# Optimization experiments

Measured on AMD Instinct MI355X. Metric: run time of the kernel, lower is better.

## Reference

```python
import jax, jax.numpy as jnp
import numpy as np

B, T, F = 16384, 48, 4
UNITS = 256
OUT_STEPS = 24


def setup_inputs() -> dict:
    key = jax.random.key(0)
    ks = jax.random.split(key, 6)
    s_x = 1.0 / np.sqrt(F)
    s_h = 1.0 / np.sqrt(UNITS)
    return {
        "x": jax.random.normal(ks[0], (B, T, F), jnp.float32),
        "Wx": jax.random.normal(ks[1], (F, 4 * UNITS), jnp.float32) * s_x,
        "Wh": jax.random.normal(ks[2], (UNITS, 4 * UNITS), jnp.float32) * s_h,
        "b": jnp.zeros((4 * UNITS,), jnp.float32),
        "Wd": jax.random.normal(ks[3], (UNITS, F), jnp.float32) * s_h,
        "bd": jnp.zeros((F,), jnp.float32),
    }


def _lstm_cell(xt, h, c, Wx, Wh, b):
    # Keras LSTMCell gate order: i, f, g(cell candidate), o
    z = xt @ Wx + h @ Wh + b  # [B, 4*units]
    i, f, g, o = jnp.split(z, 4, axis=-1)
    i = jax.nn.sigmoid(i)
    f = jax.nn.sigmoid(f)
    g = jnp.tanh(g)
    o = jax.nn.sigmoid(o)
    c_new = f * c + i * g
    h_new = o * jnp.tanh(c_new)
    return h_new, c_new


def reference(x, Wx, Wh, b, Wd, bd):
    bsz = x.shape[0]
    h0 = jnp.zeros((bsz, UNITS), x.dtype)
    c0 = jnp.zeros((bsz, UNITS), x.dtype)

    # --- warmup: run LSTM over the input window, keep final state ---
    def warm_step(carry, xt):
        h, c = carry
        h, c = _lstm_cell(xt, h, c, Wx, Wh, b)
        return (h, c), None

    (h, c), _ = jax.lax.scan(warm_step, (h0, c0), jnp.swapaxes(x, 0, 1))
    pred0 = h @ Wd + bd  # first prediction [B, F]

    def ar_step(carry, _):
        h, c, pred = carry
        h, c = _lstm_cell(pred, h, c, Wx, Wh, b)
        pred = h @ Wd + bd
        return (h, c, pred), pred

    _, preds = jax.lax.scan(ar_step, (h, c, pred0), None, length=OUT_STEPS - 1)
    preds = jnp.concatenate([pred0[None], preds], axis=0)  # [out_steps, B, F]
    return jnp.swapaxes(preds, 0, 1)  # [B, out_steps, F]
```

## Files before the change

kernel.cpp:

```cpp
#include <hip/hip_runtime.h>


typedef unsigned short u16;
typedef __attribute__((ext_vector_type(8))) short bf16x8;
typedef __attribute__((ext_vector_type(16))) float f32x16;

#define PITCH 296
#define HB 18944
#define WARM 48
#define STEPS 71
#define LOG2E  1.442695041f
#define LOG2E2 2.885390082f

__device__ __forceinline__ u16 f2bf(float f) {
    unsigned u = __float_as_uint(f);
    u += 0x7FFFu + ((u >> 16) & 1u);
    return (u16)(u >> 16);
}

__device__ __forceinline__ unsigned pk_bf16(float a, float b) {
    unsigned d;
    asm("v_cvt_pk_bf16_f32 %0, %1, %2" : "=v"(d) : "v"(a), "v"(b));
    return d;
}

__device__ __forceinline__ void sync_lds() {
    asm volatile("s_waitcnt lgkmcnt(0)\n\ts_barrier" ::: "memory");
}

__global__ void prep_weights(const float* __restrict__ Wx,
                             const float* __restrict__ Wh,
                             const float* __restrict__ b,
                             const float* __restrict__ Wd,
                             const float* __restrict__ bd,
                             u16* __restrict__ whext,
                             u16* __restrict__ wdp) {
    int idx = blockIdx.x * 256 + threadIdx.x;
    if (idx < 36864) {
        int lane = idx & 63;
        int frag = idx >> 6;
        int wv = frag & 7;
        int g = (frag >> 3) & 3;
        int kt = frag >> 5;
        int k0 = kt * 16 + (lane >> 5) * 8;
        int n = 256 * g + 32 * wv + (lane & 31);
        float sc = (g == 2) ? LOG2E2 : LOG2E;
        u16 v[8];
#pragma unroll
        for (int j = 0; j < 8; ++j) {
            int k = k0 + j;
            float f = 0.0f;
            if (k < 256) f = Wh[k * 1024 + n];
            else if (k < 260) f = Wx[(k - 256) * 1024 + n];
            else if (k == 260) f = b[n];
            v[j] = f2bf(f * sc);
        }
        ushort4* dst = (ushort4*)(whext + (size_t)idx * 8);
        dst[0] = make_ushort4(v[0], v[1], v[2], v[3]);
        dst[1] = make_ushort4(v[4], v[5], v[6], v[7]);
    } else if (idx < 36864 + 1152) {
        int id2 = idx - 36864;
        int lane = id2 & 63;
        int kt = id2 >> 6;
        int k0 = kt * 16 + (lane >> 5) * 8;
        int f_ = lane & 31;
        u16 v[8];
#pragma unroll
        for (int j = 0; j < 8; ++j) {
            int k = k0 + j;
            float f = 0.0f;
            if (f_ < 4) {
                if (k < 256) f = Wd[k * 4 + f_];
                else if (k == 260) f = bd[f_];
            }
            v[j] = f2bf(f);
        }
        ushort4* dst = (ushort4*)(wdp + (size_t)id2 * 8);
        dst[0] = make_ushort4(v[0], v[1], v[2], v[3]);
        dst[1] = make_ushort4(v[4], v[5], v[6], v[7]);
    }
}

#define WLOADT(DST, T) do {                                                   \
    const char* _wk = wp + ((size_t)(T) << 15);                               \
    _Pragma("unroll") for (int g = 0; g < 4; ++g)                             \
        DST[g] = *(const bf16x8*)(_wk + voff[g]);                             \
} while (0)

#define HLOADT(DST, T) do {                                                   \
    DST[0] = *(const bf16x8*)&hr[hrow0 + (T) * 16];                           \
    DST[1] = *(const bf16x8*)&hr[hrow1 + (T) * 16];                           \
} while (0)

#define MT(WA, HBX)                                                           \
    _Pragma("unroll") for (int m = 0; m < 2; ++m)                             \
    _Pragma("unroll") for (int g = 0; g < 4; ++g)                             \
        acc[m][g] = __builtin_amdgcn_mfma_f32_32x32x16_bf16(                  \
            WA[g], HBX[m], acc[m][g], 0, 0, 0);

__global__ __launch_bounds__(512, 2) void lstm_main(
    const float* __restrict__ x, const u16* __restrict__ whext,
    const u16* __restrict__ wdp, float* __restrict__ out) {
    __shared__ __align__(16) u16 hbuf[2 * HB];

    const int tid = threadIdx.x;
    const int w = tid >> 6;
    const int l = tid & 63;
    const int l31 = l & 31;
    const int lh = l >> 5;
    const long long rowBase = (long long)blockIdx.x * 64;

    {
        int4 z = make_int4(0, 0, 0, 0);
        for (int i = tid; i < 4736; i += 512) ((int4*)hbuf)[i] = z;
    }
    sync_lds();
    if (tid < 64) {
        hbuf[tid * PITCH + 260] = (u16)0x3F80;
        hbuf[HB + tid * PITCH + 260] = (u16)0x3F80;
        const float4 xv = *(const float4*)(x + (rowBase + tid) * 192);
        uint2* p = (uint2*)&hbuf[tid * PITCH + 256];
        *p = make_uint2(pk_bf16(xv.x, xv.y), pk_bf16(xv.z, xv.w));
    }

    const char* __restrict__ wp = (const char*)whext;
    const char* __restrict__ dp = (const char*)wdp;
    int voff[4];
#pragma unroll
    for (int g = 0; g < 4; ++g) voff[g] = ((g * 8 + w) * 64 + l) * 16;
    const int hrow0 = l31 * PITCH + lh * 8;
    const int hrow1 = (32 + l31) * PITCH + lh * 8;

    f32x16 c[2] = {};
    bf16x8 awA[4], awB[4];
    WLOADT(awA, 0);
    WLOADT(awB, 1);

    for (int step = 0; step < STEPS; ++step) {
        const u16* hr = hbuf + (step & 1) * HB;
        u16* hw = hbuf + ((step & 1) ^ 1) * HB;

        float4 xv = make_float4(0.f, 0.f, 0.f, 0.f);
        if (w == 0 && step < WARM - 1)
            xv = *(const float4*)(x + (rowBase + l) * 192 + (step + 1) * 4);

        sync_lds();

        f32x16 acc[2][4] = {};
        bf16x8 hbA[2], hbB[2];
        HLOADT(hbA, 0);
        HLOADT(hbB, 1);

#pragma unroll 1
        for (int t = 0; t < 13; t += 2) {
            MT(awA, hbA);
            WLOADT(awA, t + 2); HLOADT(hbA, t + 2);
            MT(awB, hbB);
            WLOADT(awB, t + 3); HLOADT(hbB, t + 3);
        }
        MT(awA, hbA);
        WLOADT(awA, 16); HLOADT(hbA, 16);
        MT(awB, hbB);
        WLOADT(awB, 1);
        MT(awA, hbA);
        WLOADT(awA, 0);

#pragma unroll
        for (int m = 0; m < 2; ++m) {
            const int hwrow = (32 * m + l31) * PITCH + 32 * w + 4 * lh;
#pragma unroll
            for (int q = 0; q < 4; ++q) {
                unsigned pk[2];
#pragma unroll
                for (int hp = 0; hp < 2; ++hp) {
                    float h2[2];
#pragma unroll
                    for (int rr = 0; rr < 2; ++rr) {
                        const int r = q * 4 + hp * 2 + rr;
                        float ei = __builtin_amdgcn_exp2f(-acc[m][0][r]);
                        float ef = __builtin_amdgcn_exp2f(-acc[m][1][r]);
                        float eg = __builtin_amdgcn_exp2f(-acc[m][2][r]);
                        float eo = __builtin_amdgcn_exp2f(-acc[m][3][r]);
                        float ai = 1.0f + ei, af = 1.0f + ef;
                        float ag = 1.0f + eg, ao = 1.0f + eo;
                        float P  = ai * ag;
                        float rD = __builtin_amdgcn_rcpf(P * af);
                        float cn = fmaf(c[m][r] * P, rD, (1.0f - eg) * af * rD);
                        c[m][r] = cn;
                        float ec = __builtin_amdgcn_exp2f(-LOG2E2 * cn);
                        float rE = __builtin_amdgcn_rcpf(ao * (1.0f + ec));
                        h2[rr] = (1.0f - ec) * rE;
                    }
                    pk[hp] = pk_bf16(h2[0], h2[1]);
                }
                *(uint2*)&hw[hwrow + 8 * q] = make_uint2(pk[0], pk[1]);
            }
        }

        if (step < WARM - 1) {
            if (w == 0) {
                uint2* p = (uint2*)&hw[l * PITCH + 256];
                *p = make_uint2(pk_bf16(xv.x, xv.y), pk_bf16(xv.z, xv.w));
            }
        } else {
            sync_lds();
            if (w < 2) {
                f32x16 pacc = {};
                const int prow = (32 * w + l31) * PITCH + lh * 8;
#pragma unroll
                for (int kt = 0; kt < 17; ++kt) {
                    bf16x8 hbp = *(const bf16x8*)&hw[prow + kt * 16];
                    bf16x8 wap = *(const bf16x8*)(dp + ((size_t)kt * 64 + l) * 16);
                    pacc = __builtin_amdgcn_mfma_f32_32x32x16_bf16(wap, hbp, pacc, 0, 0, 0);
                }
                if (lh == 0) {
                    int s = step - (WARM - 1);
                    int batch = 32 * w + l31;
                    *(float4*)&out[((rowBase + batch) * 24 + s) * 4] =
                        make_float4(pacc[0], pacc[1], pacc[2], pacc[3]);
                    *(uint2*)&hw[batch * PITCH + 256] =
                        make_uint2(pk_bf16(pacc[0], pacc[1]), pk_bf16(pacc[2], pacc[3]));
                }
            }
        }
    }
}

extern "C" void kernel_launch(void* const* d_in, const int* in_sizes, int n_in,
                              void* d_out, int out_size, void* d_ws, size_t ws_size,
                              hipStream_t stream) {
    const float* x  = (const float*)d_in[0];
    const float* Wx = (const float*)d_in[1];
    const float* Wh = (const float*)d_in[2];
    const float* b  = (const float*)d_in[3];
    const float* Wd = (const float*)d_in[4];
    const float* bd = (const float*)d_in[5];
    float* out = (float*)d_out;

    u16* whext = (u16*)d_ws;
    u16* wdp = (u16*)((char*)d_ws + 589824);

    prep_weights<<<(36864 + 1152 + 255) / 256, 256, 0, stream>>>(Wx, Wh, b, Wd, bd, whext, wdp);
    lstm_main<<<256, 512, 0, stream>>>(x, whext, wdp, out);
}
```

Baseline: 751.1 us.

## Triple-buffer weight fragments, make per-wave weight layout contiguous, use 16x16 MFMA for dense head

The prepared weight layout is reordered so each wave's four gate fragments for a k-tile sit contiguously, and the padded k-tiles drop from 18 to 17. The main k-loop goes from double to triple buffering of weight registers, issuing loads two stages ahead to hide global/L2 latency behind MFMAs. The output projection now uses 16x16x32 MFMAs across four waves instead of 32x32x16 across two, which cuts the wasted padded columns and the serial chain length. The third buffer adds register pressure under the 2-blocks-per-CU launch bound.

```diff
diff --git a/kernel.cpp b/kernel.cpp
--- a/kernel.cpp
+++ b/kernel.cpp
@@ -3,6 +3,7 @@
 
 typedef unsigned short u16;
 typedef __attribute__((ext_vector_type(8))) short bf16x8;
+typedef __attribute__((ext_vector_type(4))) float f32x4;
 typedef __attribute__((ext_vector_type(16))) float f32x16;
 
 #define PITCH 296
@@ -36,12 +37,12 @@
                              u16* __restrict__ whext,
                              u16* __restrict__ wdp) {
     int idx = blockIdx.x * 256 + threadIdx.x;
-    if (idx < 36864) {
+    if (idx < 34816) {
         int lane = idx & 63;
-        int frag = idx >> 6;
-        int wv = frag & 7;
-        int g = (frag >> 3) & 3;
-        int kt = frag >> 5;
+        int fr = idx >> 6;
+        int g = fr & 3;
+        int wv = (fr >> 2) & 7;
+        int kt = fr >> 5;
         int k0 = kt * 16 + (lane >> 5) * 8;
         int n = 256 * g + 32 * wv + (lane & 31);
         float sc = (g == 2) ? LOG2E2 : LOG2E;
@@ -58,20 +59,20 @@
         ushort4* dst = (ushort4*)(whext + (size_t)idx * 8);
         dst[0] = make_ushort4(v[0], v[1], v[2], v[3]);
         dst[1] = make_ushort4(v[4], v[5], v[6], v[7]);
-    } else if (idx < 36864 + 1152) {
-        int id2 = idx - 36864;
+    } else if (idx < 34816 + 576) {
+        int id2 = idx - 34816;
         int lane = id2 & 63;
-        int kt = id2 >> 6;
-        int k0 = kt * 16 + (lane >> 5) * 8;
-        int f_ = lane & 31;
+        int kc = id2 >> 6;
+        int m = lane & 15;
+        int k0 = kc * 32 + (lane >> 4) * 8;
         u16 v[8];
 #pragma unroll
         for (int j = 0; j < 8; ++j) {
             int k = k0 + j;
             float f = 0.0f;
-            if (f_ < 4) {
-                if (k < 256) f = Wd[k * 4 + f_];
-                else if (k == 260) f = bd[f_];
+            if (m < 4) {
+                if (k < 256) f = Wd[k * 4 + m];
+                else if (k == 260) f = bd[m];
             }
             v[j] = f2bf(f);
         }
@@ -81,13 +82,15 @@
     }
 }
 
-#define WLOADT(DST, T) do {                                                   \
-    const char* _wk = wp + ((size_t)(T) << 15);                               \
-    _Pragma("unroll") for (int g = 0; g < 4; ++g)                             \
-        DST[g] = *(const bf16x8*)(_wk + voff[g]);                             \
+#define WL(DST, T) do {                                                       \
+    const char* _p = wpw + ((size_t)(T) << 15);                               \
+    DST[0] = *(const bf16x8*)(_p + voffl);                                    \
+    DST[1] = *(const bf16x8*)(_p + voffl + 1024);                             \
+    DST[2] = *(const bf16x8*)(_p + voffl + 2048);                             \
+    DST[3] = *(const bf16x8*)(_p + voffl + 3072);                             \
 } while (0)
 
-#define HLOADT(DST, T) do {                                                   \
+#define HL(DST, T) do {                                                       \
     DST[0] = *(const bf16x8*)&hr[hrow0 + (T) * 16];                           \
     DST[1] = *(const bf16x8*)&hr[hrow1 + (T) * 16];                           \
 } while (0)
@@ -97,6 +100,8 @@
     _Pragma("unroll") for (int g = 0; g < 4; ++g)                             \
         acc[m][g] = __builtin_amdgcn_mfma_f32_32x32x16_bf16(                  \
             WA[g], HBX[m], acc[m][g], 0, 0, 0);
+
+#define STG(K, AW, HBX) do { MT(AW, HBX); WL(AW, (K) + 3); HL(HBX, (K) + 2); } while (0)
 
 __global__ __launch_bounds__(512, 2) void lstm_main(
     const float* __restrict__ x, const u16* __restrict__ whext,
@@ -123,18 +128,17 @@
         *p = make_uint2(pk_bf16(xv.x, xv.y), pk_bf16(xv.z, xv.w));
     }
 
-    const char* __restrict__ wp = (const char*)whext;
+    const char* __restrict__ wpw = (const char*)whext + (size_t)w * 4096;
     const char* __restrict__ dp = (const char*)wdp;
-    int voff[4];
-#pragma unroll
-    for (int g = 0; g < 4; ++g) voff[g] = ((g * 8 + w) * 64 + l) * 16;
+    const int voffl = l * 16;
     const int hrow0 = l31 * PITCH + lh * 8;
     const int hrow1 = (32 + l31) * PITCH + lh * 8;
 
     f32x16 c[2] = {};
-    bf16x8 awA[4], awB[4];
-    WLOADT(awA, 0);
-    WLOADT(awB, 1);
+    bf16x8 aw0[4], aw1[4], aw2[4];
+    WL(aw0, 0);
+    WL(aw1, 1);
+    WL(aw2, 2);
 
     for (int step = 0; step < STEPS; ++step) {
         const u16* hr = hbuf + (step & 1) * HB;
@@ -147,23 +151,24 @@
         sync_lds();
 
         f32x16 acc[2][4] = {};
-        bf16x8 hbA[2], hbB[2];
-        HLOADT(hbA, 0);
-        HLOADT(hbB, 1);
-
+        bf16x8 hb0[2], hb1[2];
+        HL(hb0, 0);
+        HL(hb1, 1);
+
+        STG(0, aw0, hb0);
+        STG(1, aw1, hb1);
 #pragma unroll 1
-        for (int t = 0; t < 13; t += 2) {
-            MT(awA, hbA);
-            WLOADT(awA, t + 2); HLOADT(hbA, t + 2);
-            MT(awB, hbB);
-            WLOADT(awB, t + 3); HLOADT(hbB, t + 3);
-        }
-        MT(awA, hbA);
-        WLOADT(awA, 16); HLOADT(hbA, 16);
-        MT(awB, hbB);
-        WLOADT(awB, 1);
-        MT(awA, hbA);
-        WLOADT(awA, 0);
+        for (int k = 2; k < 14; k += 6) {
+            STG(k + 0, aw2, hb0);
+            STG(k + 1, aw0, hb1);
+            STG(k + 2, aw1, hb0);
+            STG(k + 3, aw2, hb1);
+            STG(k + 4, aw0, hb0);
+            STG(k + 5, aw1, hb1);
+        }
+        MT(aw2, hb0); WL(aw2, 2); HL(hb0, 16);
+        MT(aw0, hb1); WL(aw0, 0);
+        MT(aw1, hb0); WL(aw1, 1);
 
 #pragma unroll
         for (int m = 0; m < 2; ++m) {
@@ -204,18 +209,19 @@
             }
         } else {
             sync_lds();
-            if (w < 2) {
-                f32x16 pacc = {};
-                const int prow = (32 * w + l31) * PITCH + lh * 8;
-#pragma unroll
-                for (int kt = 0; kt < 17; ++kt) {
-                    bf16x8 hbp = *(const bf16x8*)&hw[prow + kt * 16];
-                    bf16x8 wap = *(const bf16x8*)(dp + ((size_t)kt * 64 + l) * 16);
-                    pacc = __builtin_amdgcn_mfma_f32_32x32x16_bf16(wap, hbp, pacc, 0, 0, 0);
+            if (w < 4) {
+                f32x4 pacc = {};
+                const int col = l & 15;
+                const int prow = (16 * w + col) * PITCH + (l >> 4) * 8;
+#pragma unroll
+                for (int kc = 0; kc < 9; ++kc) {
+                    bf16x8 hbp = *(const bf16x8*)&hw[prow + kc * 32];
+                    bf16x8 wap = *(const bf16x8*)(dp + ((size_t)kc * 64 + l) * 16);
+                    pacc = __builtin_amdgcn_mfma_f32_16x16x32_bf16(wap, hbp, pacc, 0, 0, 0);
                 }
-                if (lh == 0) {
+                if ((l >> 4) == 0) {
                     int s = step - (WARM - 1);
-                    int batch = 32 * w + l31;
+                    int batch = 16 * w + col;
                     *(float4*)&out[((rowBase + batch) * 24 + s) * 4] =
                         make_float4(pacc[0], pacc[1], pacc[2], pacc[3]);
                     *(uint2*)&hw[batch * PITCH + 256] =
@@ -238,8 +244,8 @@
     float* out = (float*)d_out;
 
     u16* whext = (u16*)d_ws;
-    u16* wdp = (u16*)((char*)d_ws + 589824);
-
-    prep_weights<<<(36864 + 1152 + 255) / 256, 256, 0, stream>>>(Wx, Wh, b, Wd, bd, whext, wdp);
+    u16* wdp = (u16*)((char*)d_ws + 557056);
+
+    prep_weights<<<(34816 + 576 + 255) / 256, 256, 0, stream>>>(Wx, Wh, b, Wd, bd, whext, wdp);
     lstm_main<<<256, 512, 0, stream>>>(x, whext, wdp, out);
 }
```

New measurement: 749.1 us. About the same (-0.3%).
